# Kernel optimization log

Measured on AMD Instinct MI355X. Metric: run time of the kernel, lower is better.

The kernel has to match this reference:

```python
import jax, jax.numpy as jnp
import numpy as np

B, N, T, D = 256, 64, 60, 128
H = 128  # gate hidden dims


def setup_inputs() -> dict:
    key = jax.random.key(0)
    ks = jax.random.split(key, 5)
    x = jax.random.normal(ks[0], (B, N, T, D), dtype=jnp.float32)
    s = 1.0 / np.sqrt(D)
    sg_w1 = jax.random.normal(ks[1], (D, H), dtype=jnp.float32) * s
    sg_b1 = jnp.zeros((H,), dtype=jnp.float32)
    sg_w2 = jax.random.normal(ks[2], (H, 1), dtype=jnp.float32) * (1.0 / np.sqrt(H))
    sg_b2 = jnp.zeros((1,), dtype=jnp.float32)
    tg_w1 = jax.random.normal(ks[3], (D, H), dtype=jnp.float32) * s
    tg_b1 = jnp.zeros((H,), dtype=jnp.float32)
    tg_w2 = jax.random.normal(ks[4], (H, 1), dtype=jnp.float32) * (1.0 / np.sqrt(H))
    tg_b2 = jnp.zeros((1,), dtype=jnp.float32)
    return {"x": x, "sg_w1": sg_w1, "sg_b1": sg_b1, "sg_w2": sg_w2, "sg_b2": sg_b2,
            "tg_w1": tg_w1, "tg_b1": tg_b1, "tg_w2": tg_w2, "tg_b2": tg_b2}


def reference(x, sg_w1, sg_b1, sg_w2, sg_b2, tg_w1, tg_b1, tg_w2, tg_b2):
    # Spatial attentional aggregation, vectorized over all timesteps at once.
    # Segment softmax over batch_index == softmax over the node axis (regular segments).
    gate = jnp.tanh(x @ sg_w1 + sg_b1) @ sg_w2 + sg_b2          # [B, N, T, 1]
    alpha = jax.nn.softmax(gate, axis=1)                        # softmax over nodes
    pooled = jnp.sum(alpha * x, axis=1)                         # [B, T, D]
    # Temporal attention pooling over the sequence axis.
    score = jnp.tanh(pooled @ tg_w1 + tg_b1) @ tg_w2 + tg_b2    # [B, T, 1]
    tw = jax.nn.softmax(score, axis=1)                          # [B, T, 1]
    final = jnp.sum(tw * pooled, axis=1)                        # [B, D]
    return final, tw
```

## Files before the change

### kernel.cpp

```cpp
#include <hip/hip_runtime.h>

#define B_ 256
#define N_ 64
#define T_ 60
#define D_ 128
#define H_ 128

typedef __attribute__((ext_vector_type(8))) short short8;
typedef __attribute__((ext_vector_type(4))) float f32x4;

__device__ __forceinline__ unsigned short f2bf(float f) {
  unsigned int u = __builtin_bit_cast(unsigned int, f);
  u = u + 0x7FFFu + ((u >> 16) & 1u);
  return (unsigned short)(u >> 16);
}

__device__ __forceinline__ float tanh_fast(float x) {
  float e = __builtin_amdgcn_exp2f(x * 2.885390081777927f);
  return 1.0f - 2.0f * __builtin_amdgcn_rcpf(e + 1.0f);
}

__device__ __forceinline__ void lds_barrier() {
  asm volatile("s_waitcnt lgkmcnt(0)" ::: "memory");
  __builtin_amdgcn_s_barrier();
  asm volatile("" ::: "memory");
}

__global__ __launch_bounds__(256) void prep_weights(
    const float* __restrict__ sg_w1, const float* __restrict__ tg_w1,
    unsigned short* __restrict__ wfrag) {
  int tid = blockIdx.x * 256 + threadIdx.x;
  if (tid >= 2 * 4 * 8 * 64) return;
  int l  = tid & 63;
  int nt = (tid >> 6) & 7;
  int kt = (tid >> 9) & 3;
  int m  = tid >> 11;
  const float* W = m ? tg_w1 : sg_w1;
  int n  = nt * 16 + (l & 15);
  int k0 = kt * 32 + 8 * (l >> 4);
  unsigned short* dst = wfrag + (size_t)tid * 8;
#pragma unroll
  for (int i = 0; i < 8; ++i) dst[i] = f2bf(W[(k0 + i) * H_ + n]);
}

__global__ __launch_bounds__(256, 2) void spatial_kernel(
    const float* __restrict__ x,
    const unsigned short* __restrict__ wfrag_g,
    const float* __restrict__ b1,
    const float* __restrict__ w2,
    float* __restrict__ acc_p,
    float* __restrict__ den_p) {
  __shared__ __align__(16) char tile[64 * 272];
  __shared__ __align__(16) char wlds[32768];
  __shared__ float gpart[2][64];

  const int tid = threadIdx.x;
  const int bid = blockIdx.x;
  const int b  = bid >> 1;
  const int nh = bid & 1;

  const int sub = tid >> 5;
  const int cg  = tid & 31;

  const float* xb = x + (size_t)b * (N_ * T_ * D_) + (size_t)(nh * 32) * (T_ * D_);

  int roff[8];
#pragma unroll
  for (int r = 0; r < 8; ++r) {
    int t = 8 * r + sub;
    roff[r] = (t > 59 ? 59 : t) * D_ + 4 * cg;
  }

  const int l  = tid & 63;
  const int w  = tid >> 6;
  const int lg = l >> 4;
  const int lr = l & 15;
  const int wr = w >> 1;
  const int wc = w & 1;

  float b1v[4], w2v[4];
#pragma unroll
  for (int ntl = 0; ntl < 4; ++ntl) {
    b1v[ntl] = b1[wc * 64 + ntl * 16 + lr];
    w2v[ntl] = w2[wc * 64 + ntl * 16 + lr];
  }

  float4 wtmp[8];
#pragma unroll
  for (int i = 0; i < 8; ++i)
    wtmp[i] = *(const float4*)(wfrag_g + (size_t)(tid + 256 * i) * 8);

  float4 pxA[8], pxB[8];
#pragma unroll
  for (int r = 0; r < 8; ++r) pxA[r] = *(const float4*)(xb + roff[r]);

#pragma unroll
  for (int i = 0; i < 8; ++i)
    *(float4*)(wlds + (size_t)(tid + 256 * i) * 16) = wtmp[i];
  lds_barrier();

  f32x4 accr[8];
  float denr[8];
#pragma unroll
  for (int r = 0; r < 8; ++r) { accr[r] = (f32x4)(0.0f); denr[r] = 0.0f; }

#define SLAB_BODY(CUR, NXT, S)                                                  \
  {                                                                             \
                   \
    if ((S) < 31) {                                                             \
      const float* nsb = xb + (size_t)((S) + 1) * (T_ * D_);                    \
      _Pragma("unroll")                                                         \
      for (int r = 0; r < 8; ++r) NXT[r] = *(const float4*)(nsb + roff[r]);     \
    }                                                                           \
                                               \
    _Pragma("unroll")                                                           \
    for (int r = 0; r < 8; ++r) {                                               \
      const int t = 8 * r + sub;                                                \
      unsigned lo = ((unsigned)f2bf(CUR[r].y) << 16) | f2bf(CUR[r].x);          \
      unsigned hi = ((unsigned)f2bf(CUR[r].w) << 16) | f2bf(CUR[r].z);          \
      *(uint2*)(tile + t * 272 + cg * 8) = make_uint2(lo, hi);                  \
    }                                                                           \
    lds_barrier();                                                              \
                           \
    {                                                                           \
      f32x4 macc[2][4];                                                         \
      _Pragma("unroll")                                                         \
      for (int mt = 0; mt < 2; ++mt)                                            \
        _Pragma("unroll")                                                       \
        for (int ntl = 0; ntl < 4; ++ntl) macc[mt][ntl] = (f32x4)(0.0f);        \
      _Pragma("unroll")                                                         \
      for (int kt = 0; kt < 4; ++kt) {                                          \
        _Pragma("unroll")                                                       \
        for (int mt = 0; mt < 2; ++mt) {                                        \
          const int row = 32 * wr + 16 * mt + lr;                               \
          short8 af = *(const short8*)(tile + row * 272 + kt * 64 + lg * 16);   \
          _Pragma("unroll")                                                     \
          for (int ntl = 0; ntl < 4; ++ntl) {                                   \
            short8 bf = *(const short8*)(                                       \
                wlds + ((kt * 8 + wc * 4 + ntl) * 64 + l) * 16);                \
            macc[mt][ntl] = __builtin_amdgcn_mfma_f32_16x16x32_bf16(            \
                af, bf, macc[mt][ntl], 0, 0, 0);                                \
          }                                                                     \
        }                                                                       \
      }                                                                         \
      _Pragma("unroll")                                                         \
      for (int mt = 0; mt < 2; ++mt) {                                          \
        _Pragma("unroll")                                                       \
        for (int j = 0; j < 4; ++j) {                                           \
          float sg = 0.f;                                                       \
          _Pragma("unroll")                                                     \
          for (int ntl = 0; ntl < 4; ++ntl) {                                   \
            float h = macc[mt][ntl][j] + b1v[ntl];                              \
            sg += tanh_fast(h) * w2v[ntl];                                      \
          }                                                                     \
          sg += __shfl_xor(sg, 1);                                              \
          sg += __shfl_xor(sg, 2);                                              \
          sg += __shfl_xor(sg, 4);                                              \
          sg += __shfl_xor(sg, 8);                                              \
          if (lr == 0) gpart[wc][32 * wr + 16 * mt + 4 * lg + j] = sg;          \
        }                                                                       \
      }                                                                         \
    }                                                                           \
    lds_barrier();                                                              \
                    \
    _Pragma("unroll")                                                           \
    for (int r = 0; r < 8; ++r) {                                               \
      const int t = 8 * r + sub;                                                \
      float g = gpart[0][t] + gpart[1][t];                                      \
      float e = __builtin_amdgcn_exp2f(g * 1.4426950408889634f);                \
      accr[r][0] += e * CUR[r].x;                                               \
      accr[r][1] += e * CUR[r].y;                                               \
      accr[r][2] += e * CUR[r].z;                                               \
      accr[r][3] += e * CUR[r].w;                                               \
      denr[r] += e;                                                             \
    }                                                                           \
    lds_barrier();                                                              \
  }

  for (int sp = 0; sp < 16; ++sp) {
    const int s0 = 2 * sp;
    SLAB_BODY(pxA, pxB, s0);
    SLAB_BODY(pxB, pxA, s0 + 1);
  }
#undef SLAB_BODY

#pragma unroll
  for (int r = 0; r < 8; ++r) {
    const int t = 8 * r + sub;
    *(f32x4*)(acc_p + ((size_t)bid * 64 + t) * D_ + 4 * cg) = accr[r];
  }
  if (cg == 0) {
#pragma unroll
    for (int r = 0; r < 8; ++r) den_p[bid * 64 + 8 * r + sub] = denr[r];
  }
}

__global__ __launch_bounds__(256) void temporal_kernel(
    const float* __restrict__ acc_p,
    const float* __restrict__ den_p,
    const short8* __restrict__ wfrag,
    const float* __restrict__ b1,
    const float* __restrict__ w2,
    float* __restrict__ out) {
  __shared__ float xs[64][132];
  __shared__ float score_lds[64];
  __shared__ float tw_lds[64];
  __shared__ float pp[2][128];

  const int tid = threadIdx.x;
  const int b = blockIdx.x;

  const float* a0 = acc_p + (size_t)(2 * b) * (64 * D_);
  const float* a1 = a0 + 64 * D_;
  const float* d0 = den_p + (2 * b) * 64;
  const float* d1 = d0 + 64;
#pragma unroll
  for (int it = 0; it < 8; ++it) {
    int q = it * 256 + tid;
    int n = q >> 5;
    int c4 = (q & 31) << 2;
    float4 v = {0.f, 0.f, 0.f, 0.f};
    if (n < T_) {
      float4 v0 = *(const float4*)(a0 + n * D_ + c4);
      float4 v1 = *(const float4*)(a1 + n * D_ + c4);
      float inv = __builtin_amdgcn_rcpf(d0[n] + d1[n]);
      v.x = (v0.x + v1.x) * inv;
      v.y = (v0.y + v1.y) * inv;
      v.z = (v0.z + v1.z) * inv;
      v.w = (v0.w + v1.w) * inv;
    }
    *(float4*)(&xs[n][c4]) = v;
  }
  __syncthreads();

  const int l = tid & 63;
  const int w = tid >> 6;
  const int lg = l >> 4;
  const int lr = l & 15;

  float b1v[8], w2v[8];
#pragma unroll
  for (int nt = 0; nt < 8; ++nt) {
    b1v[nt] = b1[nt * 16 + lr];
    w2v[nt] = w2[nt * 16 + lr];
  }

  f32x4 acc[8];
#pragma unroll
  for (int nt = 0; nt < 8; ++nt) acc[nt] = (f32x4)(0.0f);

  const int row = 16 * w + lr;
#pragma unroll
  for (int kt = 0; kt < 4; ++kt) {
    const int k0 = kt * 32 + 8 * lg;
    float4 a0v = *(const float4*)(&xs[row][k0]);
    float4 a1v = *(const float4*)(&xs[row][k0 + 4]);
    short8 af;
    af[0] = (short)f2bf(a0v.x); af[1] = (short)f2bf(a0v.y);
    af[2] = (short)f2bf(a0v.z); af[3] = (short)f2bf(a0v.w);
    af[4] = (short)f2bf(a1v.x); af[5] = (short)f2bf(a1v.y);
    af[6] = (short)f2bf(a1v.z); af[7] = (short)f2bf(a1v.w);
#pragma unroll
    for (int nt = 0; nt < 8; ++nt) {
      short8 bf = wfrag[(kt * 8 + nt) * 64 + l];
      acc[nt] = __builtin_amdgcn_mfma_f32_16x16x32_bf16(af, bf, acc[nt], 0, 0, 0);
    }
  }

#pragma unroll
  for (int j = 0; j < 4; ++j) {
    float s = 0.f;
#pragma unroll
    for (int nt = 0; nt < 8; ++nt) {
      float h = acc[nt][j] + b1v[nt];
      s += tanh_fast(h) * w2v[nt];
    }
    s += __shfl_xor(s, 1);
    s += __shfl_xor(s, 2);
    s += __shfl_xor(s, 4);
    s += __shfl_xor(s, 8);
    if (lr == 0) score_lds[16 * w + 4 * lg + j] = s;
  }
  __syncthreads();

  float p = (l < T_) ? __builtin_amdgcn_exp2f(score_lds[l] * 1.4426950408889634f) : 0.f;
  float sm = p;
  sm += __shfl_xor(sm, 32);
  sm += __shfl_xor(sm, 16);
  sm += __shfl_xor(sm, 8);
  sm += __shfl_xor(sm, 4);
  sm += __shfl_xor(sm, 2);
  sm += __shfl_xor(sm, 1);
  float tw = p / sm;
  if (w == 0) {
    tw_lds[l] = tw;
    if (l < T_) out[B_ * D_ + b * T_ + l] = tw;
  }
  __syncthreads();

  const int c = tid & 127;
  const int hh = tid >> 7;
  float s = 0.f;
#pragma unroll
  for (int i = 0; i < 30; ++i) {
    int tt = 30 * hh + i;
    s += tw_lds[tt] * xs[tt][c];
  }
  pp[hh][c] = s;
  __syncthreads();
  if (tid < 128) out[(size_t)b * D_ + tid] = pp[0][tid] + pp[1][tid];
}

extern "C" void kernel_launch(void* const* d_in, const int* in_sizes, int n_in,
                              void* d_out, int out_size, void* d_ws, size_t ws_size,
                              hipStream_t stream) {
  const float* x     = (const float*)d_in[0];
  const float* sg_w1 = (const float*)d_in[1];
  const float* sg_b1 = (const float*)d_in[2];
  const float* sg_w2 = (const float*)d_in[3];
  const float* tg_w1 = (const float*)d_in[5];
  const float* tg_b1 = (const float*)d_in[6];
  const float* tg_w2 = (const float*)d_in[7];
  float* out = (float*)d_out;

  unsigned short* wfrag = (unsigned short*)d_ws;
  float* acc_p = (float*)((char*)d_ws + 65536);
  float* den_p = (float*)((char*)d_ws + 65536 + 16777216);

  prep_weights<<<16, 256, 0, stream>>>(sg_w1, tg_w1, wfrag);
  spatial_kernel<<<B_ * 2, 256, 0, stream>>>(
      x, wfrag, sg_b1, sg_w2, acc_p, den_p);
  temporal_kernel<<<B_, 256, 0, stream>>>(
      acc_p, den_p, (const short8*)(wfrag + 16384), tg_b1, tg_w2, out);
}
```

Baseline: 145.0 us.

## Split spatial kernel over time halves to double block count

The spatial kernel now partitions each batch's work into four blocks (node half times time half) instead of two. Each block handles 32 timestep rows per slab, which halves per-block registers, LDS tile size and MFMA work per iteration. The temporal kernel's gather of partial sums is changed to match the new layout. This gives more parallelism across CUs (1024 blocks instead of 512) at the cost of each block reloading the weight fragments into LDS and paying more barriers per useful work.

```diff
diff --git a/kernel.cpp b/kernel.cpp
--- a/kernel.cpp
+++ b/kernel.cpp
@@ -50,25 +50,28 @@
     const float* __restrict__ w2,
     float* __restrict__ acc_p,
     float* __restrict__ den_p) {
-  __shared__ __align__(16) char tile[64 * 272];
+  __shared__ __align__(16) char tile[32 * 272];
   __shared__ __align__(16) char wlds[32768];
-  __shared__ float gpart[2][64];
+  __shared__ float gpart[2][32];
 
   const int tid = threadIdx.x;
   const int bid = blockIdx.x;
-  const int b  = bid >> 1;
-  const int nh = bid & 1;
+  const int b  = bid >> 2;
+  const int nh = (bid >> 1) & 1;
+  const int th = bid & 1;
 
   const int sub = tid >> 5;
   const int cg  = tid & 31;
 
-  const float* xb = x + (size_t)b * (N_ * T_ * D_) + (size_t)(nh * 32) * (T_ * D_);
-
-  int roff[8];
-#pragma unroll
-  for (int r = 0; r < 8; ++r) {
-    int t = 8 * r + sub;
-    roff[r] = (t > 59 ? 59 : t) * D_ + 4 * cg;
+  const float* xb = x + (size_t)b * (N_ * T_ * D_)
+                      + (size_t)(nh * 32) * (T_ * D_) + (size_t)(th * 32) * D_;
+
+  const int rmax = th ? 27 : 31;
+  int roff[4];
+#pragma unroll
+  for (int j = 0; j < 4; ++j) {
+    int r = 8 * j + sub;
+    roff[j] = (r > rmax ? rmax : r) * D_ + 4 * cg;
   }
 
   const int l  = tid & 63;
@@ -90,19 +93,19 @@
   for (int i = 0; i < 8; ++i)
     wtmp[i] = *(const float4*)(wfrag_g + (size_t)(tid + 256 * i) * 8);
 
-  float4 pxA[8], pxB[8];
-#pragma unroll
-  for (int r = 0; r < 8; ++r) pxA[r] = *(const float4*)(xb + roff[r]);
+  float4 pxA[4], pxB[4];
+#pragma unroll
+  for (int j = 0; j < 4; ++j) pxA[j] = *(const float4*)(xb + roff[j]);
 
 #pragma unroll
   for (int i = 0; i < 8; ++i)
     *(float4*)(wlds + (size_t)(tid + 256 * i) * 16) = wtmp[i];
   lds_barrier();
 
-  f32x4 accr[8];
-  float denr[8];
-#pragma unroll
-  for (int r = 0; r < 8; ++r) { accr[r] = (f32x4)(0.0f); denr[r] = 0.0f; }
+  f32x4 accr[4];
+  float denr[4];
+#pragma unroll
+  for (int j = 0; j < 4; ++j) { accr[j] = (f32x4)(0.0f); denr[j] = 0.0f; }
 
 #define SLAB_BODY(CUR, NXT, S)                                                  \
   {                                                                             \
@@ -110,69 +113,62 @@
     if ((S) < 31) {                                                             \
       const float* nsb = xb + (size_t)((S) + 1) * (T_ * D_);                    \
       _Pragma("unroll")                                                         \
-      for (int r = 0; r < 8; ++r) NXT[r] = *(const float4*)(nsb + roff[r]);     \
+      for (int j = 0; j < 4; ++j) NXT[j] = *(const float4*)(nsb + roff[j]);     \
     }                                                                           \
-                                               \
+                                 \
     _Pragma("unroll")                                                           \
-    for (int r = 0; r < 8; ++r) {                                               \
-      const int t = 8 * r + sub;                                                \
-      unsigned lo = ((unsigned)f2bf(CUR[r].y) << 16) | f2bf(CUR[r].x);          \
-      unsigned hi = ((unsigned)f2bf(CUR[r].w) << 16) | f2bf(CUR[r].z);          \
-      *(uint2*)(tile + t * 272 + cg * 8) = make_uint2(lo, hi);                  \
+    for (int j = 0; j < 4; ++j) {                                               \
+      const int r = 8 * j + sub;                                                \
+      unsigned lo = ((unsigned)f2bf(CUR[j].y) << 16) | f2bf(CUR[j].x);          \
+      unsigned hi = ((unsigned)f2bf(CUR[j].w) << 16) | f2bf(CUR[j].z);          \
+      *(uint2*)(tile + r * 272 + cg * 8) = make_uint2(lo, hi);                  \
     }                                                                           \
     lds_barrier();                                                              \
-                           \
+               \
     {                                                                           \
-      f32x4 macc[2][4];                                                         \
+      f32x4 macc[4];                                                            \
       _Pragma("unroll")                                                         \
-      for (int mt = 0; mt < 2; ++mt)                                            \
-        _Pragma("unroll")                                                       \
-        for (int ntl = 0; ntl < 4; ++ntl) macc[mt][ntl] = (f32x4)(0.0f);        \
+      for (int ntl = 0; ntl < 4; ++ntl) macc[ntl] = (f32x4)(0.0f);              \
       _Pragma("unroll")                                                         \
       for (int kt = 0; kt < 4; ++kt) {                                          \
+        const int row = 16 * wr + lr;                                           \
+        short8 af = *(const short8*)(tile + row * 272 + kt * 64 + lg * 16);     \
         _Pragma("unroll")                                                       \
-        for (int mt = 0; mt < 2; ++mt) {                                        \
-          const int row = 32 * wr + 16 * mt + lr;                               \
-          short8 af = *(const short8*)(tile + row * 272 + kt * 64 + lg * 16);   \
-          _Pragma("unroll")                                                     \
-          for (int ntl = 0; ntl < 4; ++ntl) {                                   \
-            short8 bf = *(const short8*)(                                       \
-                wlds + ((kt * 8 + wc * 4 + ntl) * 64 + l) * 16);                \
-            macc[mt][ntl] = __builtin_amdgcn_mfma_f32_16x16x32_bf16(            \
-                af, bf, macc[mt][ntl], 0, 0, 0);                                \
-          }                                                                     \
+        for (int ntl = 0; ntl < 4; ++ntl) {                                     \
+          short8 bf = *(const short8*)(                                         \
+              wlds + ((kt * 8 + wc * 4 + ntl) * 64 + l) * 16);                  \
+          macc[ntl] = __builtin_amdgcn_mfma_f32_16x16x32_bf16(                  \
+              af, bf, macc[ntl], 0, 0, 0);                                      \
         }                                                                       \
       }                                                                         \
+                               \
       _Pragma("unroll")                                                         \
-      for (int mt = 0; mt < 2; ++mt) {                                          \
+      for (int j = 0; j < 4; ++j) {                                             \
+        float sg = 0.f;                                                         \
         _Pragma("unroll")                                                       \
-        for (int j = 0; j < 4; ++j) {                                           \
-          float sg = 0.f;                                                       \
-          _Pragma("unroll")                                                     \
-          for (int ntl = 0; ntl < 4; ++ntl) {                                   \
-            float h = macc[mt][ntl][j] + b1v[ntl];                              \
-            sg += tanh_fast(h) * w2v[ntl];                                      \
-          }                                                                     \
-          sg += __shfl_xor(sg, 1);                                              \
-          sg += __shfl_xor(sg, 2);                                              \
-          sg += __shfl_xor(sg, 4);                                              \
-          sg += __shfl_xor(sg, 8);                                              \
-          if (lr == 0) gpart[wc][32 * wr + 16 * mt + 4 * lg + j] = sg;          \
+        for (int ntl = 0; ntl < 4; ++ntl) {                                     \
+          float h = macc[ntl][j] + b1v[ntl];                                    \
+          sg += tanh_fast(h) * w2v[ntl];                                        \
         }                                                                       \
+        sg += __shfl_xor(sg, 1);                                                \
+        sg += __shfl_xor(sg, 2);                                                \
+        sg += __shfl_xor(sg, 4);                                                \
+        sg += __shfl_xor(sg, 8);                                                \
+        if (lr == 0) gpart[wc][16 * wr + 4 * lg + j] = sg;                      \
       }                                                                         \
     }                                                                           \
     lds_barrier();                                                              \
                     \
     _Pragma("unroll")                                                           \
-    for (int r = 0; r < 8; ++r) {                                               \
-      const int t = 8 * r + sub;                                                \
-      float g = gpart[0][t] + gpart[1][t];                                      \
+    for (int j = 0; j < 4; ++j) {                                               \
+      const int r = 8 * j + sub;                                                \
+      float g = gpart[0][r] + gpart[1][r];                                      \
       float e = __builtin_amdgcn_exp2f(g * 1.4426950408889634f);                \
-      accr[r][0] += e * CUR[r].x;                                               \
-      accr[r][1] += e * CUR[r].y;                                               \
-      accr[r][2] += e * CUR[r].z;                                               \
-      accr[r][3] += e * CUR[r].w;                                               \
-      denr[r] += e;                                                             \
+      accr[j][0] += e * CUR[j].x;                                               \
+      accr[j][1] += e * CUR[j].y;                                               \
+      accr[j][2] += e * CUR[j].z;                                               \
+      accr[j][3] += e * CUR[j].w;                                               \
+      denr[j] += e;                                                             \
     }                                                                           \
     lds_barrier();                                                              \
   }
@@ -185,13 +181,13 @@
 #undef SLAB_BODY
 
 #pragma unroll
-  for (int r = 0; r < 8; ++r) {
-    const int t = 8 * r + sub;
-    *(f32x4*)(acc_p + ((size_t)bid * 64 + t) * D_ + 4 * cg) = accr[r];
+  for (int j = 0; j < 4; ++j) {
+    const int r = 8 * j + sub;
+    *(f32x4*)(acc_p + ((size_t)bid * 32 + r) * D_ + 4 * cg) = accr[j];
   }
   if (cg == 0) {
 #pragma unroll
-    for (int r = 0; r < 8; ++r) den_p[bid * 64 + 8 * r + sub] = denr[r];
+    for (int j = 0; j < 4; ++j) den_p[bid * 32 + 8 * j + sub] = denr[j];
   }
 }
 
@@ -210,10 +206,6 @@
   const int tid = threadIdx.x;
   const int b = blockIdx.x;
 
-  const float* a0 = acc_p + (size_t)(2 * b) * (64 * D_);
-  const float* a1 = a0 + 64 * D_;
-  const float* d0 = den_p + (2 * b) * 64;
-  const float* d1 = d0 + 64;
 #pragma unroll
   for (int it = 0; it < 8; ++it) {
     int q = it * 256 + tid;
@@ -221,9 +213,13 @@
     int c4 = (q & 31) << 2;
     float4 v = {0.f, 0.f, 0.f, 0.f};
     if (n < T_) {
-      float4 v0 = *(const float4*)(a0 + n * D_ + c4);
-      float4 v1 = *(const float4*)(a1 + n * D_ + c4);
-      float inv = __builtin_amdgcn_rcpf(d0[n] + d1[n]);
+      int thh = n >> 5, tl = n & 31;
+      const float* a0 = acc_p + ((size_t)(b * 4 + thh) * 32 + tl) * D_;
+      const float* a1 = acc_p + ((size_t)(b * 4 + 2 + thh) * 32 + tl) * D_;
+      float4 v0 = *(const float4*)(a0 + c4);
+      float4 v1 = *(const float4*)(a1 + c4);
+      float inv = __builtin_amdgcn_rcpf(den_p[(b * 4 + thh) * 32 + tl] +
+                                        den_p[(b * 4 + 2 + thh) * 32 + tl]);
       v.x = (v0.x + v1.x) * inv;
       v.y = (v0.y + v1.y) * inv;
       v.z = (v0.z + v1.z) * inv;
@@ -328,7 +324,7 @@
   float* den_p = (float*)((char*)d_ws + 65536 + 16777216);
 
   prep_weights<<<16, 256, 0, stream>>>(sg_w1, tg_w1, wfrag);
-  spatial_kernel<<<B_ * 2, 256, 0, stream>>>(
+  spatial_kernel<<<B_ * 4, 256, 0, stream>>>(
       x, wfrag, sg_b1, sg_w2, acc_p, den_p);
   temporal_kernel<<<B_, 256, 0, stream>>>(
       acc_p, den_p, (const short8*)(wfrag + 16384), tg_b1, tg_w2, out);
```

Result: no change. 142.5 us (-1.7%).
